# Optimization experiments

Hardware: AMD Instinct MI355X
Metric: run time of the kernel (lower is better)

Reference implementation:

```python
import jax, jax.numpy as jnp
import numpy as np

TQ, TV, B, D, UNITS = 256, 1024, 4, 128, 128
NEG_INF = -1e9


def setup_inputs() -> dict:
    key = jax.random.key(0)
    k1, k2, k3, k4, k5, k6 = jax.random.split(key, 6)
    query = jax.random.normal(k1, (TQ, B, D), dtype=jnp.float32)
    value = jax.random.normal(k2, (TV, B, D), dtype=jnp.float32)
    mask = jax.random.randint(k3, (TV, B), 0, 2).astype(bool)
    # guarantee at least one valid key position per batch element
    mask = mask.at[0].set(True)
    # Dense kernels (glorot-uniform-like scaled normals are fine for a reference)
    W1 = jax.random.normal(k4, (D, UNITS), dtype=jnp.float32) * (1.0 / np.sqrt(D))
    W2 = jax.random.normal(k5, (D, UNITS), dtype=jnp.float32) * (1.0 / np.sqrt(D))
    # AdditiveAttention use_scale=True -> learnable scale vector of shape (units,)
    scale = jax.random.normal(k6, (UNITS,), dtype=jnp.float32) * (1.0 / np.sqrt(UNITS))
    return {"query": query, "value": value, "mask": mask, "W1": W1, "W2": W2, "scale": scale}


def reference(query, value, mask, W1, W2, scale):
    # time-major -> batch-major
    q = jnp.transpose(query, (1, 0, 2))   # [B, Tq, D]
    v = jnp.transpose(value, (1, 0, 2))   # [B, Tv, D]
    m = jnp.transpose(mask, (1, 0))       # [B, Tv] bool (value mask)

    wq = jnp.einsum('bqd,du->bqu', q, W1)  # [B, Tq, U]
    wk = jnp.einsum('bvd,du->bvu', v, W2)  # [B, Tv, U]

    # additive score: sum_u scale[u] * tanh(wq[b,q,u] + wk[b,v,u]) -> [B, Tq, Tv]
    scores = jnp.einsum('u,bqvu->bqv', scale, jnp.tanh(wq[:, :, None, :] + wk[:, None, :, :]))

    scores = jnp.where(m[:, None, :], scores, NEG_INF)
    attn = jax.nn.softmax(scores, axis=-1)          # [B, Tq, Tv]
    ctx = jnp.einsum('bqv,bvd->bqd', attn, v)       # [B, Tq, D]

    # batch-major -> time-major
    return jnp.transpose(ctx, (1, 0, 2))            # [Tq, B, D]
```

## Files before the change

kernel.cpp:

```cpp
#include <hip/hip_runtime.h>


#define TQ 256
#define TV 1024
#define BB 4
#define DD 128
#define UU 128
#define NEG_INF -1e9f
#define C2LOG2E 2.8853900817779268f

union SharedA {
  struct { float Wl[DD * UU]; float xs[8][DD]; } pj;
  struct { int wsum[4]; float sred[2]; } cp;
};

__global__ __launch_bounds__(256) void prep_kernel(
    const float* __restrict__ query, const float* __restrict__ value,
    const float* __restrict__ W1, const float* __restrict__ W2,
    const int* __restrict__ mask, const float* __restrict__ scale,
    float* __restrict__ Eq, float* __restrict__ Ek,
    int* __restrict__ valid_idx, int* __restrict__ nvalid,
    float* __restrict__ Ssum)
{
  __shared__ SharedA u;
  const int t = threadIdx.x, lane = t & 63, wid = t >> 6;
  const int bid = blockIdx.x;

  if (bid < BB) {
    const int b = bid;
    int m[4];
#pragma unroll
    for (int k = 0; k < 4; ++k) m[k] = mask[(4 * t + k) * BB + b] ? 1 : 0;
    int cnt = m[0] + m[1] + m[2] + m[3];
    int pre = cnt;
#pragma unroll
    for (int off = 1; off < 64; off <<= 1) {
      int y = __shfl_up(pre, off, 64);
      if (lane >= off) pre += y;
    }
    if (lane == 63) u.cp.wsum[wid] = pre;
    float sv_ = (t < UU) ? scale[t] : 0.f;
#pragma unroll
    for (int off = 32; off > 0; off >>= 1) sv_ += __shfl_xor(sv_, off, 64);
    if (t == 0)  u.cp.sred[0] = sv_;
    if (t == 64) u.cp.sred[1] = sv_;
    __syncthreads();
    int base = 0;
#pragma unroll
    for (int w = 0; w < 4; ++w) if (w < wid) base += u.cp.wsum[w];
    int total = u.cp.wsum[0] + u.cp.wsum[1] + u.cp.wsum[2] + u.cp.wsum[3];
    int idx = base + pre - cnt;
#pragma unroll
    for (int k = 0; k < 4; ++k)
      if (m[k]) valid_idx[b * TV + (idx++)] = 4 * t + k;
    for (int i = t; i < TV; i += 256)
      if (i >= total) valid_idx[b * TV + i] = 0;
    if (t == 0) nvalid[b] = total;
    if (b == 0 && t == 0) Ssum[0] = u.cp.sred[0] + u.cp.sred[1];
  } else {
    const int blk = bid - BB;
    const bool isq = blk < (TQ * BB / 8);
    const float* X = isq ? query : value;
    const float* W = isq ? W1 : W2;
    float* E       = isq ? Eq : Ek;
    const int T    = isq ? TQ : TV;
    const int R0   = (isq ? blk : blk - TQ * BB / 8) * 8;

    const float4* Wg = (const float4*)W;
    float4* Wl4 = (float4*)u.pj.Wl;
#pragma unroll
    for (int k = 0; k < 16; ++k)
      Wl4[k * 256 + t] = Wg[k * 256 + t];
    ((float4*)u.pj.xs)[t] = ((const float4*)(X + (size_t)R0 * DD))[t];
    __syncthreads();

    const int half = t >> 7;
    const int uu_ = t & 127;
    float a[4] = {0.f, 0.f, 0.f, 0.f};
#pragma unroll 4
    for (int d = 0; d < DD; ++d) {
      float wv = u.pj.Wl[d * UU + uu_];
#pragma unroll
      for (int i = 0; i < 4; ++i)
        a[i] += u.pj.xs[half * 4 + i][d] * wv;
    }
#pragma unroll
    for (int i = 0; i < 4; ++i) {
      int rf = R0 + half * 4 + i;
      int b2 = rf & (BB - 1), tt = rf >> 2;
      E[((size_t)b2 * T + tt) * UU + uu_] =
          __builtin_amdgcn_exp2f(a[i] * C2LOG2E);
    }
  }
}

#define QUAD(Av, Kv, acc)                                          \
  { float d0 = __builtin_fmaf(Av.x, Kv.x, 1.f);                    \
    float d1 = __builtin_fmaf(Av.y, Kv.y, 1.f);                    \
    float d2 = __builtin_fmaf(Av.z, Kv.z, 1.f);                    \
    float d3 = __builtin_fmaf(Av.w, Kv.w, 1.f);                    \
    float m01 = d0 * d1, m23 = d2 * d3;                            \
    float R = __builtin_amdgcn_rcpf(m01 * m23);                    \
    float q01 = R * m23, q23 = R * m01;                            \
    acc = __builtin_fmaf(sv.x, q01 * d1, acc);                     \
    acc = __builtin_fmaf(sv.y, q01 * d0, acc);                     \
    acc = __builtin_fmaf(sv.z, q23 * d3, acc);                     \
    acc = __builtin_fmaf(sv.w, q23 * d2, acc); }

__global__ __launch_bounds__(256, 4) void scores_kernel(
    const float* __restrict__ Eq,
    const float* __restrict__ Ek,
    const float* __restrict__ scale,
    const float* __restrict__ Ssum,
    const int*   __restrict__ valid_idx,
    const int*   __restrict__ nvalid,
    float* __restrict__ scores)
{
  const int b  = blockIdx.z;
  const int nv = nvalid[b];
  const int v0 = blockIdx.x * 64;
  if (v0 >= nv) return;
  const int q0 = blockIdx.y * 16;
  const int t  = threadIdx.x;

  __shared__ float4 eq_lds[16 * 32];
  __shared__ float4 ek_lds[64 * 32];
  __shared__ int    vidx[64];

  if (t < 64) vidx[t] = valid_idx[b * TV + v0 + t];
  {
    const float4* gq = (const float4*)Eq + ((size_t)(b * TQ + q0)) * 32;
    eq_lds[t]       = gq[t];
    eq_lds[256 + t] = gq[256 + t];
  }
  __syncthreads();
  {
    const float4* gk = (const float4*)Ek;
#pragma unroll
    for (int k = 0; k < 8; ++k) {
      int i = k * 256 + t;
      int r = i >> 5, c = i & 31;
      ek_lds[r * 32 + (c ^ (r & 7))] =
          gk[((size_t)(b * TV + vidx[r])) * 32 + c];
    }
  }
  __syncthreads();

  const int qp = t >> 5;
  const int vp = t & 31;
  const int sx = vp & 7;
  const float4* Ar0 = eq_lds + (2 * qp) * 32;
  const float4* Ar1 = Ar0 + 32;
  const float4* Kr0 = ek_lds + vp * 32;
  const float4* Kr1 = ek_lds + (vp + 32) * 32;
  const float4* S4  = (const float4*)scale;

  float a00 = 0.f, a01 = 0.f, a10 = 0.f, a11 = 0.f;
#pragma unroll 8
  for (int uu = 0; uu < 32; ++uu) {
    float4 A0 = Ar0[uu];
    float4 A1 = Ar1[uu];
    int cs = uu ^ sx;
    float4 K0 = Kr0[cs];
    float4 K1 = Kr1[cs];
    float4 sv = S4[uu];
    QUAD(A0, K0, a00)
    QUAD(A0, K1, a01)
    QUAD(A1, K0, a10)
    QUAD(A1, K1, a11)
  }
  const float S = Ssum[0];
  float* row0 = scores + ((size_t)(b * TQ + q0 + 2 * qp)) * TV + v0;
  row0[vp]           = __builtin_fmaf(-2.f, a00, S);
  row0[vp + 32]      = __builtin_fmaf(-2.f, a01, S);
  row0[TV + vp]      = __builtin_fmaf(-2.f, a10, S);
  row0[TV + vp + 32] = __builtin_fmaf(-2.f, a11, S);
}

__global__ __launch_bounds__(512) void softmax_ctx_kernel(
    const float* __restrict__ value,
    const int*   __restrict__ valid_idx,
    const int*   __restrict__ nvalid,
    const float* __restrict__ scores,
    float* __restrict__ out)
{
  const int bi = blockIdx.x;
  const int b  = bi >> 6;
  const int q0 = (bi & 63) * 4;
  const int nv = nvalid[b];
  const int t = threadIdx.x, lane = t & 63;

  __shared__ float p_lds[4][TV];
  __shared__ int   vidx[TV];
  __shared__ float redm[4][2];
  __shared__ float reds[4][2];
  __shared__ float part[3][4][DD];

  if (t < 256) ((int4*)vidx)[t] = ((const int4*)(valid_idx + b * TV))[t];

  const int j = t >> 7;
  const int c = t & 127;
  const int wslot = (t >> 6) & 1;

  const float* srow = scores + ((size_t)(b * TQ + q0 + j)) * TV;
  float4 x0 = ((const float4*)srow)[c];
  float4 x1 = ((const float4*)srow)[c + 128];
  const int e0 = 4 * c, e1 = 512 + 4 * c;
  x0.x = (e0 + 0 < nv) ? x0.x : NEG_INF;
  x0.y = (e0 + 1 < nv) ? x0.y : NEG_INF;
  x0.z = (e0 + 2 < nv) ? x0.z : NEG_INF;
  x0.w = (e0 + 3 < nv) ? x0.w : NEG_INF;
  x1.x = (e1 + 0 < nv) ? x1.x : NEG_INF;
  x1.y = (e1 + 1 < nv) ? x1.y : NEG_INF;
  x1.z = (e1 + 2 < nv) ? x1.z : NEG_INF;
  x1.w = (e1 + 3 < nv) ? x1.w : NEG_INF;

  float mm = fmaxf(fmaxf(fmaxf(x0.x, x0.y), fmaxf(x0.z, x0.w)),
                   fmaxf(fmaxf(x1.x, x1.y), fmaxf(x1.z, x1.w)));
#pragma unroll
  for (int off = 32; off > 0; off >>= 1)
    mm = fmaxf(mm, __shfl_xor(mm, off, 64));
  if (lane == 0) redm[j][wslot] = mm;
  __syncthreads();
  mm = fmaxf(redm[j][0], redm[j][1]);

  float4 p0, p1;
  p0.x = __expf(x0.x - mm); p0.y = __expf(x0.y - mm);
  p0.z = __expf(x0.z - mm); p0.w = __expf(x0.w - mm);
  p1.x = __expf(x1.x - mm); p1.y = __expf(x1.y - mm);
  p1.z = __expf(x1.z - mm); p1.w = __expf(x1.w - mm);
  ((float4*)&p_lds[j][0])[c]       = p0;
  ((float4*)&p_lds[j][0])[c + 128] = p1;

  float ss = ((p0.x + p0.y) + (p0.z + p0.w)) +
             ((p1.x + p1.y) + (p1.z + p1.w));
#pragma unroll
  for (int off = 32; off > 0; off >>= 1)
    ss += __shfl_xor(ss, off, 64);
  if (lane == 0) reds[j][wslot] = ss;
  __syncthreads();

  const int qtr = t >> 7;
  const int d = t & 127;
  const int nChunks = (nv + 3) >> 2;
  float a0 = 0.f, a1 = 0.f, a2 = 0.f, a3 = 0.f;
  const float* vbase = value + b * DD + d;
  for (int ch = qtr; ch < nChunks; ch += 4) {
    int4 id = ((const int4*)vidx)[ch];
    float4 q0v = ((const float4*)&p_lds[0][0])[ch];
    float4 q1v = ((const float4*)&p_lds[1][0])[ch];
    float4 q2v = ((const float4*)&p_lds[2][0])[ch];
    float4 q3v = ((const float4*)&p_lds[3][0])[ch];
    float v0_ = vbase[(size_t)id.x * (BB * DD)];
    float v1_ = vbase[(size_t)id.y * (BB * DD)];
    float v2_ = vbase[(size_t)id.z * (BB * DD)];
    float v3_ = vbase[(size_t)id.w * (BB * DD)];
    a0 = __builtin_fmaf(q0v.x, v0_, a0); a0 = __builtin_fmaf(q0v.y, v1_, a0);
    a0 = __builtin_fmaf(q0v.z, v2_, a0); a0 = __builtin_fmaf(q0v.w, v3_, a0);
    a1 = __builtin_fmaf(q1v.x, v0_, a1); a1 = __builtin_fmaf(q1v.y, v1_, a1);
    a1 = __builtin_fmaf(q1v.z, v2_, a1); a1 = __builtin_fmaf(q1v.w, v3_, a1);
    a2 = __builtin_fmaf(q2v.x, v0_, a2); a2 = __builtin_fmaf(q2v.y, v1_, a2);
    a2 = __builtin_fmaf(q2v.z, v2_, a2); a2 = __builtin_fmaf(q2v.w, v3_, a2);
    a3 = __builtin_fmaf(q3v.x, v0_, a3); a3 = __builtin_fmaf(q3v.y, v1_, a3);
    a3 = __builtin_fmaf(q3v.z, v2_, a3); a3 = __builtin_fmaf(q3v.w, v3_, a3);
  }
  if (qtr) {
    part[qtr - 1][0][d] = a0;
    part[qtr - 1][1][d] = a1;
    part[qtr - 1][2][d] = a2;
    part[qtr - 1][3][d] = a3;
  }
  __syncthreads();
  if (qtr == 0) {
    float tot[4] = {a0, a1, a2, a3};
#pragma unroll
    for (int jj = 0; jj < 4; ++jj) {
      float s = tot[jj] + part[0][jj][d] + part[1][jj][d] + part[2][jj][d];
      float iv = 1.f / (reds[jj][0] + reds[jj][1]);
      out[((size_t)(q0 + jj) * BB + b) * DD + d] = s * iv;
    }
  }
}

extern "C" void kernel_launch(void* const* d_in, const int* in_sizes, int n_in,
                              void* d_out, int out_size, void* d_ws, size_t ws_size,
                              hipStream_t stream) {
  const float* query = (const float*)d_in[0];
  const float* value = (const float*)d_in[1];
  const int*   mask  = (const int*)  d_in[2];
  const float* W1    = (const float*)d_in[3];
  const float* W2    = (const float*)d_in[4];
  const float* scale = (const float*)d_in[5];
  float* out = (float*)d_out;

  float* Eq      = (float*)d_ws;
  float* Ek      = Eq + (size_t)BB * TQ * UU;
  float* scores  = Ek + (size_t)BB * TV * UU;
  int*   vidx    = (int*)(scores + (size_t)BB * TQ * TV);
  int*   nvalid  = vidx + BB * TV;
  float* Ssum    = (float*)(nvalid + BB);

  prep_kernel<<<BB + (TQ + TV) * BB / 8, 256, 0, stream>>>(
      query, value, W1, W2, mask, scale, Eq, Ek, vidx, nvalid, Ssum);
  scores_kernel<<<dim3(TV / 64, TQ / 16, BB), 256, 0, stream>>>(
      Eq, Ek, scale, Ssum, vidx, nvalid, scores);
  softmax_ctx_kernel<<<BB * TQ / 4, 512, 0, stream>>>(
      value, vidx, nvalid, scores, out);
}
```

Baseline: 45.08 us.

## Fuse score computation with softmax and context into one kernel

```diff
diff --git a/kernel.cpp b/kernel.cpp
--- a/kernel.cpp
+++ b/kernel.cpp
@@ -8,6 +8,19 @@
 #define UU 128
 #define NEG_INF -1e9f
 #define C2LOG2E 2.8853900817779268f
+
+#define QUAD1(Av, Kv, sv, acc)                                     \
+  { float d0 = __builtin_fmaf(Av.x, Kv.x, 1.f);                    \
+    float d1 = __builtin_fmaf(Av.y, Kv.y, 1.f);                    \
+    float d2 = __builtin_fmaf(Av.z, Kv.z, 1.f);                    \
+    float d3 = __builtin_fmaf(Av.w, Kv.w, 1.f);                    \
+    float m01 = d0 * d1, m23 = d2 * d3;                            \
+    float R = __builtin_amdgcn_rcpf(m01 * m23);                    \
+    float q01 = R * m23, q23 = R * m01;                            \
+    acc = __builtin_fmaf(sv.x, q01 * d1, acc);                     \
+    acc = __builtin_fmaf(sv.y, q01 * d0, acc);                     \
+    acc = __builtin_fmaf(sv.z, q23 * d3, acc);                     \
+    acc = __builtin_fmaf(sv.w, q23 * d2, acc); }
 
 union SharedA {
   struct { float Wl[DD * UU]; float xs[8][DD]; } pj;
@@ -94,191 +107,137 @@
   }
 }
 
-#define QUAD(Av, Kv, acc)                                          \
-  { float d0 = __builtin_fmaf(Av.x, Kv.x, 1.f);                    \
-    float d1 = __builtin_fmaf(Av.y, Kv.y, 1.f);                    \
-    float d2 = __builtin_fmaf(Av.z, Kv.z, 1.f);                    \
-    float d3 = __builtin_fmaf(Av.w, Kv.w, 1.f);                    \
-    float m01 = d0 * d1, m23 = d2 * d3;                            \
-    float R = __builtin_amdgcn_rcpf(m01 * m23);                    \
-    float q01 = R * m23, q23 = R * m01;                            \
-    acc = __builtin_fmaf(sv.x, q01 * d1, acc);                     \
-    acc = __builtin_fmaf(sv.y, q01 * d0, acc);                     \
-    acc = __builtin_fmaf(sv.z, q23 * d3, acc);                     \
-    acc = __builtin_fmaf(sv.w, q23 * d2, acc); }
-
-__global__ __launch_bounds__(256, 4) void scores_kernel(
+__global__ __launch_bounds__(512, 1) void attn_kernel(
+    const float* __restrict__ value,
     const float* __restrict__ Eq,
     const float* __restrict__ Ek,
     const float* __restrict__ scale,
     const float* __restrict__ Ssum,
     const int*   __restrict__ valid_idx,
     const int*   __restrict__ nvalid,
-    float* __restrict__ scores)
-{
-  const int b  = blockIdx.z;
-  const int nv = nvalid[b];
-  const int v0 = blockIdx.x * 64;
-  if (v0 >= nv) return;
-  const int q0 = blockIdx.y * 16;
-  const int t  = threadIdx.x;
-
-  __shared__ float4 eq_lds[16 * 32];
-  __shared__ float4 ek_lds[64 * 32];
-  __shared__ int    vidx[64];
-
-  if (t < 64) vidx[t] = valid_idx[b * TV + v0 + t];
-  {
-    const float4* gq = (const float4*)Eq + ((size_t)(b * TQ + q0)) * 32;
-    eq_lds[t]       = gq[t];
-    eq_lds[256 + t] = gq[256 + t];
-  }
-  __syncthreads();
-  {
-    const float4* gk = (const float4*)Ek;
-#pragma unroll
-    for (int k = 0; k < 8; ++k) {
-      int i = k * 256 + t;
-      int r = i >> 5, c = i & 31;
-      ek_lds[r * 32 + (c ^ (r & 7))] =
-          gk[((size_t)(b * TV + vidx[r])) * 32 + c];
-    }
-  }
-  __syncthreads();
-
-  const int qp = t >> 5;
-  const int vp = t & 31;
-  const int sx = vp & 7;
-  const float4* Ar0 = eq_lds + (2 * qp) * 32;
-  const float4* Ar1 = Ar0 + 32;
-  const float4* Kr0 = ek_lds + vp * 32;
-  const float4* Kr1 = ek_lds + (vp + 32) * 32;
-  const float4* S4  = (const float4*)scale;
-
-  float a00 = 0.f, a01 = 0.f, a10 = 0.f, a11 = 0.f;
-#pragma unroll 8
-  for (int uu = 0; uu < 32; ++uu) {
-    float4 A0 = Ar0[uu];
-    float4 A1 = Ar1[uu];
-    int cs = uu ^ sx;
-    float4 K0 = Kr0[cs];
-    float4 K1 = Kr1[cs];
-    float4 sv = S4[uu];
-    QUAD(A0, K0, a00)
-    QUAD(A0, K1, a01)
-    QUAD(A1, K0, a10)
-    QUAD(A1, K1, a11)
-  }
-  const float S = Ssum[0];
-  float* row0 = scores + ((size_t)(b * TQ + q0 + 2 * qp)) * TV + v0;
-  row0[vp]           = __builtin_fmaf(-2.f, a00, S);
-  row0[vp + 32]      = __builtin_fmaf(-2.f, a01, S);
-  row0[TV + vp]      = __builtin_fmaf(-2.f, a10, S);
-  row0[TV + vp + 32] = __builtin_fmaf(-2.f, a11, S);
-}
-
-__global__ __launch_bounds__(512) void softmax_ctx_kernel(
-    const float* __restrict__ value,
-    const int*   __restrict__ valid_idx,
-    const int*   __restrict__ nvalid,
-    const float* __restrict__ scores,
     float* __restrict__ out)
 {
-  const int bi = blockIdx.x;
-  const int b  = bi >> 6;
-  const int q0 = (bi & 63) * 4;
-  const int nv = nvalid[b];
-  const int t = threadIdx.x, lane = t & 63;
-
-  __shared__ float p_lds[4][TV];
-  __shared__ int   vidx[TV];
-  __shared__ float redm[4][2];
-  __shared__ float reds[4][2];
-  __shared__ float part[3][4][DD];
+  const int bid = blockIdx.x;
+  const int b   = bid >> 6;
+  const int q0  = (bid & 63) * 4;
+  const int t   = threadIdx.x;
+  const int lane = t & 63;
+
+  __shared__ float4 kv_lds[128 * 32];
+  __shared__ float  s_lds[4][TV];
+  __shared__ float4 eq_lds[4 * 32];
+  __shared__ int    vidx[TV];
+  __shared__ float  redm[4][2], redsum[4][2], inv_s[4];
+  __shared__ float  part[4][64][2];
+
+  const int nv  = nvalid[b];
+  const int nvt = (nv + 127) >> 7;
+  const float S = Ssum[0];
 
   if (t < 256) ((int4*)vidx)[t] = ((const int4*)(valid_idx + b * TV))[t];
-
-  const int j = t >> 7;
-  const int c = t & 127;
+  if (t < 128) eq_lds[t] = ((const float4*)Eq)[((size_t)(b * TQ + q0)) * 32 + t];
+  __syncthreads();
+
+  const int q  = t >> 7;
+  const int vl = t & 127;
+  const int sx = vl & 7;
+  const float4* S4 = (const float4*)scale;
+
+  for (int tix = 0; tix < nvt; ++tix) {
+    if (tix) __syncthreads();
+    {
+      const float4* gk = (const float4*)Ek;
+#pragma unroll
+      for (int k = 0; k < 8; ++k) {
+        int i = k * 512 + t;
+        int r = i >> 5, c = i & 31;
+        kv_lds[r * 32 + (c ^ (r & 7))] =
+            gk[((size_t)(b * TV + vidx[tix * 128 + r])) * 32 + c];
+      }
+    }
+    __syncthreads();
+
+    const float4* Ar = eq_lds + q * 32;
+    const float4* Kr = kv_lds + vl * 32;
+    float acc = 0.f;
+#pragma unroll 8
+    for (int uu = 0; uu < 32; ++uu) {
+      float4 A0 = Ar[uu];
+      float4 K0 = Kr[uu ^ sx];
+      float4 sv = S4[uu];
+      QUAD1(A0, K0, sv, acc)
+    }
+    s_lds[q][tix * 128 + vl] = __builtin_fmaf(-2.f, acc, S);
+  }
+  __syncthreads();
+
   const int wslot = (t >> 6) & 1;
-
-  const float* srow = scores + ((size_t)(b * TQ + q0 + j)) * TV;
-  float4 x0 = ((const float4*)srow)[c];
-  float4 x1 = ((const float4*)srow)[c + 128];
-  const int e0 = 4 * c, e1 = 512 + 4 * c;
-  x0.x = (e0 + 0 < nv) ? x0.x : NEG_INF;
-  x0.y = (e0 + 1 < nv) ? x0.y : NEG_INF;
-  x0.z = (e0 + 2 < nv) ? x0.z : NEG_INF;
-  x0.w = (e0 + 3 < nv) ? x0.w : NEG_INF;
-  x1.x = (e1 + 0 < nv) ? x1.x : NEG_INF;
-  x1.y = (e1 + 1 < nv) ? x1.y : NEG_INF;
-  x1.z = (e1 + 2 < nv) ? x1.z : NEG_INF;
-  x1.w = (e1 + 3 < nv) ? x1.w : NEG_INF;
-
-  float mm = fmaxf(fmaxf(fmaxf(x0.x, x0.y), fmaxf(x0.z, x0.w)),
-                   fmaxf(fmaxf(x1.x, x1.y), fmaxf(x1.z, x1.w)));
+  float mm = NEG_INF;
+#pragma unroll
+  for (int k = 0; k < 8; ++k) {
+    int gv = vl + 128 * k;
+    float x = (gv < nv) ? s_lds[q][gv] : NEG_INF;
+    mm = fmaxf(mm, x);
+  }
 #pragma unroll
   for (int off = 32; off > 0; off >>= 1)
     mm = fmaxf(mm, __shfl_xor(mm, off, 64));
-  if (lane == 0) redm[j][wslot] = mm;
-  __syncthreads();
-  mm = fmaxf(redm[j][0], redm[j][1]);
-
-  float4 p0, p1;
-  p0.x = __expf(x0.x - mm); p0.y = __expf(x0.y - mm);
-  p0.z = __expf(x0.z - mm); p0.w = __expf(x0.w - mm);
-  p1.x = __expf(x1.x - mm); p1.y = __expf(x1.y - mm);
-  p1.z = __expf(x1.z - mm); p1.w = __expf(x1.w - mm);
-  ((float4*)&p_lds[j][0])[c]       = p0;
-  ((float4*)&p_lds[j][0])[c + 128] = p1;
-
-  float ss = ((p0.x + p0.y) + (p0.z + p0.w)) +
-             ((p1.x + p1.y) + (p1.z + p1.w));
+  if (lane == 0) redm[q][wslot] = mm;
+  __syncthreads();
+  mm = fmaxf(redm[q][0], redm[q][1]);
+
+  float ssum = 0.f;
+#pragma unroll
+  for (int k = 0; k < 8; ++k) {
+    int gv = vl + 128 * k;
+    float x = (gv < nv) ? s_lds[q][gv] : NEG_INF;
+    float p = __expf(x - mm);
+    s_lds[q][gv] = p;
+    ssum += p;
+  }
 #pragma unroll
   for (int off = 32; off > 0; off >>= 1)
-    ss += __shfl_xor(ss, off, 64);
-  if (lane == 0) reds[j][wslot] = ss;
-  __syncthreads();
-
-  const int qtr = t >> 7;
-  const int d = t & 127;
-  const int nChunks = (nv + 3) >> 2;
-  float a0 = 0.f, a1 = 0.f, a2 = 0.f, a3 = 0.f;
-  const float* vbase = value + b * DD + d;
-  for (int ch = qtr; ch < nChunks; ch += 4) {
-    int4 id = ((const int4*)vidx)[ch];
-    float4 q0v = ((const float4*)&p_lds[0][0])[ch];
-    float4 q1v = ((const float4*)&p_lds[1][0])[ch];
-    float4 q2v = ((const float4*)&p_lds[2][0])[ch];
-    float4 q3v = ((const float4*)&p_lds[3][0])[ch];
-    float v0_ = vbase[(size_t)id.x * (BB * DD)];
-    float v1_ = vbase[(size_t)id.y * (BB * DD)];
-    float v2_ = vbase[(size_t)id.z * (BB * DD)];
-    float v3_ = vbase[(size_t)id.w * (BB * DD)];
-    a0 = __builtin_fmaf(q0v.x, v0_, a0); a0 = __builtin_fmaf(q0v.y, v1_, a0);
-    a0 = __builtin_fmaf(q0v.z, v2_, a0); a0 = __builtin_fmaf(q0v.w, v3_, a0);
-    a1 = __builtin_fmaf(q1v.x, v0_, a1); a1 = __builtin_fmaf(q1v.y, v1_, a1);
-    a1 = __builtin_fmaf(q1v.z, v2_, a1); a1 = __builtin_fmaf(q1v.w, v3_, a1);
-    a2 = __builtin_fmaf(q2v.x, v0_, a2); a2 = __builtin_fmaf(q2v.y, v1_, a2);
-    a2 = __builtin_fmaf(q2v.z, v2_, a2); a2 = __builtin_fmaf(q2v.w, v3_, a2);
-    a3 = __builtin_fmaf(q3v.x, v0_, a3); a3 = __builtin_fmaf(q3v.y, v1_, a3);
-    a3 = __builtin_fmaf(q3v.z, v2_, a3); a3 = __builtin_fmaf(q3v.w, v3_, a3);
-  }
-  if (qtr) {
-    part[qtr - 1][0][d] = a0;
-    part[qtr - 1][1][d] = a1;
-    part[qtr - 1][2][d] = a2;
-    part[qtr - 1][3][d] = a3;
-  }
-  __syncthreads();
-  if (qtr == 0) {
-    float tot[4] = {a0, a1, a2, a3};
-#pragma unroll
-    for (int jj = 0; jj < 4; ++jj) {
-      float s = tot[jj] + part[0][jj][d] + part[1][jj][d] + part[2][jj][d];
-      float iv = 1.f / (reds[jj][0] + reds[jj][1]);
-      out[((size_t)(q0 + jj) * BB + b) * DD + d] = s * iv;
-    }
+    ssum += __shfl_xor(ssum, off, 64);
+  if (lane == 0) redsum[q][wslot] = ssum;
+  __syncthreads();
+  if (t < 4) inv_s[t] = 1.f / (redsum[t][0] + redsum[t][1]);
+
+  const int vh = (t >> 6) & 1;
+  const int dp = t & 63;
+  float ax = 0.f, ay = 0.f;
+
+  for (int tix = 0; tix < nvt; ++tix) {
+    __syncthreads();
+    {
+      const float4* gv4 = (const float4*)value;
+#pragma unroll
+      for (int k = 0; k < 8; ++k) {
+        int i = k * 512 + t;
+        int r = i >> 5, c = i & 31;
+        kv_lds[r * 32 + c] =
+            gv4[((size_t)vidx[tix * 128 + r] * BB + b) * 32 + c];
+      }
+    }
+    __syncthreads();
+
+    const float* Vl = (const float*)kv_lds;
+    const int lim = min(128, nv - tix * 128);
+    const float* prow = &s_lds[q][tix * 128];
+    for (int v = vh; v < lim; v += 2) {
+      float p = prow[v];
+      float2 vv = *(const float2*)(Vl + v * 128 + 2 * dp);
+      ax = __builtin_fmaf(p, vv.x, ax);
+      ay = __builtin_fmaf(p, vv.y, ay);
+    }
+  }
+
+  if (vh) { part[q][dp][0] = ax; part[q][dp][1] = ay; }
+  __syncthreads();
+  if (!vh) {
+    float iv = inv_s[q];
+    float2 o = make_float2((ax + part[q][dp][0]) * iv,
+                           (ay + part[q][dp][1]) * iv);
+    *(float2*)&out[((size_t)(q0 + q) * BB + b) * DD + 2 * dp] = o;
   }
 }
 
@@ -295,15 +254,12 @@
 
   float* Eq      = (float*)d_ws;
   float* Ek      = Eq + (size_t)BB * TQ * UU;
-  float* scores  = Ek + (size_t)BB * TV * UU;
-  int*   vidx    = (int*)(scores + (size_t)BB * TQ * TV);
+  int*   vidx    = (int*)(Ek + (size_t)BB * TV * UU);
   int*   nvalid  = vidx + BB * TV;
   float* Ssum    = (float*)(nvalid + BB);
 
   prep_kernel<<<BB + (TQ + TV) * BB / 8, 256, 0, stream>>>(
       query, value, W1, W2, mask, scale, Eq, Ek, vidx, nvalid, Ssum);
-  scores_kernel<<<dim3(TV / 64, TQ / 16, BB), 256, 0, stream>>>(
-      Eq, Ek, scale, Ssum, vidx, nvalid, scores);
-  softmax_ctx_kernel<<<BB * TQ / 4, 512, 0, stream>>>(
-      value, vidx, nvalid, scores, out);
+  attn_kernel<<<BB * TQ / 4, 512, 0, stream>>>(
+      value, Eq, Ek, scale, Ssum, vidx, nvalid, out);
 }
```

Result: slower. 55.73 us (+23.6%).
